# Kernel optimization log

Hardware: AMD Instinct MI355X
Metric: run time of the kernel (lower is better)

Reference implementation:

```python
import math
import jax, jax.numpy as jnp
import numpy as np

SPECIAL = 4; LABEL_ID = 3
ACT_V = 64; TIME_V = 32
VOCAB = SPECIAL + ACT_V + TIME_V  # 100
D = 1024; L = 4; H = 16; DH = D // H
B = 4; T = 1024
CAT0, CAT1 = 16, 32
N_NUM = 4; N_TIME = 6


def _posenc(t, d):
    pos = np.arange(t)[:, None]
    i = np.arange(d // 2)[None, :]
    ang = pos / np.power(10000.0, 2.0 * i / d)
    pe = np.zeros((t, d), dtype=np.float32)
    pe[:, 0::2] = np.sin(ang)
    pe[:, 1::2] = np.cos(ang)
    return jnp.asarray(pe)


def _ln(x, g, b):
    m = jnp.mean(x, -1, keepdims=True)
    v = jnp.mean((x - m) ** 2, -1, keepdims=True)
    return (x - m) * jax.lax.rsqrt(v + 1e-5) * g + b


def setup_inputs() -> dict:
    key = jax.random.key(0)
    ks = iter(jax.random.split(key, 64))
    nrm = lambda shape, s=0.02: jax.random.normal(next(ks), shape, jnp.float32) * s
    inp = {}
    inp['tokens'] = jax.random.randint(next(ks), (B, T), 0, VOCAB)
    inp['cat_feats'] = jax.random.randint(next(ks), (B, T, 2), 0, CAT0)
    inp['num_feats'] = jax.random.normal(next(ks), (B, T, N_NUM), jnp.float32)
    inp['time_feats'] = jax.random.normal(next(ks), (B, T, N_TIME), jnp.float32)
    inp['attention_mask'] = jnp.ones((B, T), jnp.int32)
    inp['loss_mask'] = jax.random.randint(next(ks), (B, T), 0, 2).astype(bool)
    inp['task_ids'] = jax.random.randint(next(ks), (B,), 0, 2)
    # embedder params
    inp['E'] = nrm((VOCAB, D))
    inp['cat_emb0'] = nrm((CAT0, D))
    inp['cat_emb1'] = nrm((CAT1, D))
    inp['Wn'] = nrm((N_NUM, D)); inp['bn'] = jnp.zeros((D,), jnp.float32)
    inp['Wt'] = nrm((N_TIME, D)); inp['bt'] = jnp.zeros((D,), jnp.float32)
    # backbone params, stacked over layers
    inp['Wqkv'] = nrm((L, D, 3 * D)); inp['bqkv'] = jnp.zeros((L, 3 * D), jnp.float32)
    inp['Wo'] = nrm((L, D, D)); inp['bo'] = jnp.zeros((L, D), jnp.float32)
    inp['ln1_g'] = jnp.ones((L, D), jnp.float32); inp['ln1_b'] = jnp.zeros((L, D), jnp.float32)
    inp['W1'] = nrm((L, D, 4 * D)); inp['b1'] = jnp.zeros((L, 4 * D), jnp.float32)
    inp['W2'] = nrm((L, 4 * D, D)); inp['b2'] = jnp.zeros((L, D), jnp.float32)
    inp['ln2_g'] = jnp.ones((L, D), jnp.float32); inp['ln2_b'] = jnp.zeros((L, D), jnp.float32)
    inp['lnf_g'] = jnp.ones((D,), jnp.float32); inp['lnf_b'] = jnp.zeros((D,), jnp.float32)
    # heads
    inp['W_next'] = nrm((D, ACT_V)); inp['b_next'] = jnp.zeros((ACT_V,), jnp.float32)
    inp['W_timeh'] = nrm((D, TIME_V)); inp['b_timeh'] = jnp.zeros((TIME_V,), jnp.float32)
    inp['task_embed'] = nrm((2, D))
    inp['tied_scale_act'] = jnp.asarray(0.5, jnp.float32)
    inp['tied_scale_time'] = jnp.asarray(0.5, jnp.float32)
    inp['copy_scale_act'] = jnp.asarray(0.5, jnp.float32)
    inp['copy_scale_time'] = jnp.asarray(0.5, jnp.float32)
    return inp


def reference(tokens, cat_feats, num_feats, time_feats, attention_mask, loss_mask, task_ids,
              E, cat_emb0, cat_emb1, Wn, bn, Wt, bt,
              Wqkv, bqkv, Wo, bo, ln1_g, ln1_b, W1, b1, W2, b2, ln2_g, ln2_b, lnf_g, lnf_b,
              W_next, b_next, W_timeh, b_timeh, task_embed,
              tied_scale_act, tied_scale_time, copy_scale_act, copy_scale_time):
    Bq, Tq = tokens.shape
    # ---- EventEmbedder: sum of token/categorical/numeric/time embeddings + PE
    x = E[tokens] + cat_emb0[cat_feats[..., 0]] + cat_emb1[cat_feats[..., 1]]
    x = x + num_feats @ Wn + bn + time_feats @ Wt + bt
    x = x + _posenc(Tq, D)
    # ---- task conditioning
    x = x + task_embed[task_ids][:, None, :]
    # ---- causal + key-padding mask
    pad = attention_mask == 0
    causal = jnp.triu(jnp.ones((Tq, Tq), bool), 1)
    neg = jnp.where(causal[None, None] | pad[:, None, None, :], -1e9, 0.0).astype(x.dtype)
    # ---- pre-LN decoder-only transformer
    for l in range(L):
        hln = _ln(x, ln1_g[l], ln1_b[l])
        qkv = hln @ Wqkv[l] + bqkv[l]
        q, k, v = jnp.split(qkv, 3, axis=-1)
        q = q.reshape(Bq, Tq, H, DH); k = k.reshape(Bq, Tq, H, DH); v = v.reshape(Bq, Tq, H, DH)
        sc = jnp.einsum('bqhd,bkhd->bhqk', q, k) / math.sqrt(DH) + neg
        p = jax.nn.softmax(sc, axis=-1)
        a = jnp.einsum('bhqk,bkhd->bqhd', p, v).reshape(Bq, Tq, D)
        x = x + a @ Wo[l] + bo[l]
        hln = _ln(x, ln2_g[l], ln2_b[l])
        x = x + jax.nn.relu(hln @ W1[l] + b1[l]) @ W2[l] + b2[l]
    h = _ln(x, lnf_g, lnf_b)  # [B,T,D]
    # ---- parametric heads
    param_next = h @ W_next + b_next
    param_time = h @ W_timeh + b_timeh
    # ---- weight-tied heads
    W_act = E[SPECIAL:SPECIAL + ACT_V]
    W_tb = E[SPECIAL + ACT_V:SPECIAL + ACT_V + TIME_V]
    tied_act = h @ W_act.T
    tied_time = h @ W_tb.T
    # ---- retrieval/copy head (vectorized gather-matmul-scatter)
    is_label = tokens == LABEL_ID
    value_mask = jnp.pad(is_label[:, :-1], ((0, 0), (1, 0)))  # prev token is <LABEL>
    act_start = SPECIAL; time_start = SPECIAL + ACT_V
    val_act = value_mask & (tokens >= act_start) & (tokens < time_start)
    val_time = value_mask & (tokens >= time_start) & (tokens < time_start + TIME_V)
    sims = jnp.einsum('bqd,bkd->bqk', h, h) / math.sqrt(D)  # all-pairs similarity
    oh_act = jax.nn.one_hot(tokens - act_start, ACT_V, dtype=h.dtype) * val_act[..., None]
    oh_time = jax.nn.one_hot(tokens - time_start, TIME_V, dtype=h.dtype) * val_time[..., None]
    qm = loss_mask[..., None].astype(h.dtype)  # copy logits only at query <LABEL> positions
    copy_act = jnp.einsum('bqk,bkc->bqc', sims, oh_act) * qm
    copy_time = jnp.einsum('bqk,bkc->bqc', sims, oh_time) * qm
    sp = jax.nn.softplus
    activity_logits = param_next + sp(tied_scale_act) * tied_act + sp(copy_scale_act) * copy_act
    time_logits = param_time + sp(tied_scale_time) * tied_time + sp(copy_scale_time) * copy_time
    return activity_logits, time_logits
```

## Files before the change

### kernel.cpp

```cpp
#include <hip/hip_runtime.h>
#include <cstdint>
#include <cstddef>

typedef unsigned short u16;
typedef __attribute__((ext_vector_type(8))) short bf16x8;
typedef __attribute__((ext_vector_type(4))) float f32x4;

#define DMODEL 1024
#define TLEN   1024
#define BATCH  4
#define NHEAD  16

__device__ __forceinline__ float bf2f(u16 u) {
  union { unsigned int i; float f; } x; x.i = ((unsigned int)u) << 16; return x.f;
}
__device__ __forceinline__ u16 f2bf(float f) {
  union { float f; unsigned int i; } x; x.f = f;
  unsigned int r = x.i + 0x7fffu + ((x.i >> 16) & 1u);
  return (u16)(r >> 16);
}
__device__ __forceinline__ void ld8bf(const u16* p, float* f) {
  uint4 u = *(const uint4*)p;
  f[0] = bf2f((u16)(u.x & 0xffff)); f[1] = bf2f((u16)(u.x >> 16));
  f[2] = bf2f((u16)(u.y & 0xffff)); f[3] = bf2f((u16)(u.y >> 16));
  f[4] = bf2f((u16)(u.z & 0xffff)); f[5] = bf2f((u16)(u.z >> 16));
  f[6] = bf2f((u16)(u.w & 0xffff)); f[7] = bf2f((u16)(u.w >> 16));
}
__device__ __forceinline__ void ld4bf(const u16* p, float* f) {
  uint2 u = *(const uint2*)p;
  f[0] = bf2f((u16)(u.x & 0xffff)); f[1] = bf2f((u16)(u.x >> 16));
  f[2] = bf2f((u16)(u.y & 0xffff)); f[3] = bf2f((u16)(u.y >> 16));
}
__device__ __forceinline__ float softplus_f(float x) {
  return (x > 20.f) ? x : log1pf(__expf(x));
}
__device__ __forceinline__ void async_ld16(const void* g, void* l) {
  __builtin_amdgcn_global_load_lds(
      (const __attribute__((address_space(1))) unsigned int*)g,
      (__attribute__((address_space(3))) unsigned int*)l, 16, 0, 0);
}

__global__ void embed_kernel(const int* __restrict__ tokens, const int* __restrict__ cat,
    const float* __restrict__ numf, const float* __restrict__ timef, const int* __restrict__ task_ids,
    const float* __restrict__ E, const float* __restrict__ ce0, const float* __restrict__ ce1,
    const float* __restrict__ Wn, const float* __restrict__ bn, const float* __restrict__ Wtm,
    const float* __restrict__ btm, const float* __restrict__ taskemb, float* __restrict__ X)
{
  const int bt = blockIdx.x;
  const int b = bt >> 10, t = bt & 1023;
  const int tok = tokens[bt];
  const int c0 = cat[bt * 2 + 0], c1 = cat[bt * 2 + 1];
  const int tk = task_ids[b];
  float nf[4], tf[6];
#pragma unroll
  for (int i = 0; i < 4; ++i) nf[i] = numf[bt * 4 + i];
#pragma unroll
  for (int i = 0; i < 6; ++i) tf[i] = timef[bt * 6 + i];
  const int d0 = threadIdx.x * 4;
  float v[4];
  {
    float4 a = *(const float4*)(E + (size_t)tok * DMODEL + d0);
    float4 b2 = *(const float4*)(ce0 + (size_t)c0 * DMODEL + d0);
    float4 c2 = *(const float4*)(ce1 + (size_t)c1 * DMODEL + d0);
    float4 d2 = *(const float4*)(taskemb + (size_t)tk * DMODEL + d0);
    float4 e2 = *(const float4*)(bn + d0);
    float4 f2 = *(const float4*)(btm + d0);
    v[0] = a.x + b2.x + c2.x + d2.x + e2.x + f2.x;
    v[1] = a.y + b2.y + c2.y + d2.y + e2.y + f2.y;
    v[2] = a.z + b2.z + c2.z + d2.z + e2.z + f2.z;
    v[3] = a.w + b2.w + c2.w + d2.w + e2.w + f2.w;
  }
#pragma unroll
  for (int i = 0; i < 4; ++i) {
    float4 w = *(const float4*)(Wn + (size_t)i * DMODEL + d0);
    v[0] += nf[i] * w.x; v[1] += nf[i] * w.y; v[2] += nf[i] * w.z; v[3] += nf[i] * w.w;
  }
#pragma unroll
  for (int i = 0; i < 6; ++i) {
    float4 w = *(const float4*)(Wtm + (size_t)i * DMODEL + d0);
    v[0] += tf[i] * w.x; v[1] += tf[i] * w.y; v[2] += tf[i] * w.z; v[3] += tf[i] * w.w;
  }
#pragma unroll
  for (int j = 0; j < 4; ++j) {
    const int d = d0 + j;
    const int i2 = d >> 1;
    const float ang = (float)t * expf(-0.017988946f * (float)i2);
    v[j] += (d & 1) ? cosf(ang) : sinf(ang);
  }
  *(float4*)(X + (size_t)bt * DMODEL + d0) = make_float4(v[0], v[1], v[2], v[3]);
}

__global__ void ln_kernel(const float* __restrict__ X, const float* __restrict__ g,
                          const float* __restrict__ be, u16* __restrict__ O)
{
  const int row = blockIdx.x * 4 + (threadIdx.x >> 6);
  const int lane = threadIdx.x & 63;
  const float* xr = X + (size_t)row * DMODEL;
  float v[16];
  float s = 0.f, s2 = 0.f;
#pragma unroll
  for (int i = 0; i < 4; ++i) {
    float4 t4 = *(const float4*)(xr + lane * 4 + i * 256);
    v[i*4+0] = t4.x; v[i*4+1] = t4.y; v[i*4+2] = t4.z; v[i*4+3] = t4.w;
    s  += t4.x + t4.y + t4.z + t4.w;
    s2 += t4.x*t4.x + t4.y*t4.y + t4.z*t4.z + t4.w*t4.w;
  }
#pragma unroll
  for (int off = 32; off > 0; off >>= 1) {
    s  += __shfl_xor(s, off, 64);
    s2 += __shfl_xor(s2, off, 64);
  }
  const float mean = s * (1.f / 1024.f);
  const float var  = s2 * (1.f / 1024.f) - mean * mean;
  const float rs   = rsqrtf(var + 1e-5f);
  u16* orow = O + (size_t)row * DMODEL;
#pragma unroll
  for (int i = 0; i < 4; ++i) {
    float4 gg = *(const float4*)(g + lane * 4 + i * 256);
    float4 bb = *(const float4*)(be + lane * 4 + i * 256);
    float r0 = (v[i*4+0] - mean) * rs * gg.x + bb.x;
    float r1 = (v[i*4+1] - mean) * rs * gg.y + bb.y;
    float r2 = (v[i*4+2] - mean) * rs * gg.z + bb.z;
    float r3 = (v[i*4+3] - mean) * rs * gg.w + bb.w;
    uint2 o2;
    o2.x = (unsigned)f2bf(r0) | ((unsigned)f2bf(r1) << 16);
    o2.y = (unsigned)f2bf(r2) | ((unsigned)f2bf(r3) << 16);
    *(uint2*)(orow + lane * 4 + i * 256) = o2;
  }
}

__global__ void transpose_f2b(const float* __restrict__ in, u16* __restrict__ out,
                              int R, int C, int ldin)
{
  __shared__ u16 tile[64][65];
  const int c0 = blockIdx.x * 64, r0 = blockIdx.y * 64;
  const int tx = threadIdx.x & 15, ty = threadIdx.x >> 4;
#pragma unroll
  for (int i = 0; i < 4; ++i) {
    const int r = ty + i * 16;
    float4 f = *(const float4*)(in + (size_t)(r0 + r) * ldin + c0 + tx * 4);
    tile[r][tx*4+0] = f2bf(f.x);
    tile[r][tx*4+1] = f2bf(f.y);
    tile[r][tx*4+2] = f2bf(f.z);
    tile[r][tx*4+3] = f2bf(f.w);
  }
  __syncthreads();
#pragma unroll
  for (int i = 0; i < 4; ++i) {
    const int rr = ty + i * 16;
    uint2 o;
    o.x = (unsigned)tile[tx*4+0][rr] | ((unsigned)tile[tx*4+1][rr] << 16);
    o.y = (unsigned)tile[tx*4+2][rr] | ((unsigned)tile[tx*4+3][rr] << 16);
    *(uint2*)(out + (size_t)(c0 + rr) * R + r0 + tx * 4) = o;
  }
}

template<bool RESID, bool RELU, bool OUTBF>
__global__ void gemm_bt(const u16* __restrict__ A, const u16* __restrict__ Bt,
                        const float* __restrict__ bias, const float* __restrict__ resid,
                        void* __restrict__ outp, int M, int N, int K, int lda)
{
  __shared__ u16 As[128 * 32];
  __shared__ u16 Bs[128 * 32];
  const int tid = threadIdx.x;
  const int wave = tid >> 6, lane = tid & 63;
  const int m0 = blockIdx.y * 128, n0 = blockIdx.x * 128;
  const int wm = (wave >> 1) * 64, wn = (wave & 1) * 64;
  const int lrow = lane & 15, quad = lane >> 4;
  f32x4 acc[4][4] = {};
  for (int kt = 0; kt < K; kt += 32) {
    __syncthreads();
#pragma unroll
    for (int p = 0; p < 2; ++p) {
      const int idx = p * 256 + tid;
      const int r = idx >> 2, cc = (idx & 3) << 3;
      const int lofs = (p * 256 + wave * 64) << 3;
      async_ld16(A + (size_t)(m0 + r) * lda + kt + cc, As + lofs);
      async_ld16(Bt + (size_t)(n0 + r) * K + kt + cc, Bs + lofs);
    }
    __syncthreads();
    bf16x8 af[4], bfr[4];
#pragma unroll
    for (int i = 0; i < 4; ++i) {
      af[i]  = *(const bf16x8*)(As + (wm + i * 16 + lrow) * 32 + quad * 8);
      bfr[i] = *(const bf16x8*)(Bs + (wn + i * 16 + lrow) * 32 + quad * 8);
    }
#pragma unroll
    for (int i = 0; i < 4; ++i)
#pragma unroll
      for (int j = 0; j < 4; ++j)
        acc[i][j] = __builtin_amdgcn_mfma_f32_16x16x32_bf16(af[i], bfr[j], acc[i][j], 0, 0, 0);
  }
#pragma unroll
  for (int i = 0; i < 4; ++i) {
#pragma unroll
    for (int j = 0; j < 4; ++j) {
      const int col = n0 + wn + j * 16 + lrow;
      const float bv = bias ? bias[col] : 0.f;
#pragma unroll
      for (int r = 0; r < 4; ++r) {
        const int row = m0 + wm + i * 16 + quad * 4 + r;
        float vv = acc[i][j][r] + bv;
        if (RESID) vv += resid[(size_t)row * N + col];
        if (RELU)  vv = fmaxf(vv, 0.f);
        if (OUTBF) ((u16*)outp)[(size_t)row * N + col] = f2bf(vv);
        else       ((float*)outp)[(size_t)row * N + col] = vv;
      }
    }
  }
}

__launch_bounds__(256, 4)
__global__ void attn_flash(u16* __restrict__ QKV, const int* __restrict__ amask)
{
  __shared__ u16 Pw[4][16 * 72];
  const int tid  = threadIdx.x;
  const int wave = tid >> 6, lane = tid & 63;
  const int l15  = lane & 15, quad = lane >> 4;
  const int qb = blockIdx.x, h = blockIdx.y, b = blockIdx.z;
  const int qbase = qb * 64 + wave * 16;

  u16* bq = QKV + (size_t)b * TLEN * 3072 + h * 64;
  const u16* Kb = bq + 1024;
  const u16* Vb = bq + 2048;
  const int* am = amask + b * TLEN;

  bf16x8 aq0 = *(const bf16x8*)(bq + (size_t)(qbase + l15) * 3072 + quad * 8);
  bf16x8 aq1 = *(const bf16x8*)(bq + (size_t)(qbase + l15) * 3072 + 32 + quad * 8);

  f32x4 o[4] = {};
  float m[4], l[4];
#pragma unroll
  for (int r = 0; r < 4; ++r) { m[r] = -1e30f; l[r] = 0.f; }

  u16* myP = Pw[wave];

  for (int kb = 0; kb <= qb; ++kb) {
    const int kt = kb * 64;
    float p[4][4];
#pragma unroll
    for (int j = 0; j < 4; ++j) {
      const u16* kr = Kb + (size_t)(kt + j * 16 + l15) * 3072;
      bf16x8 bk0 = *(const bf16x8*)(kr + quad * 8);
      bf16x8 bk1 = *(const bf16x8*)(kr + 32 + quad * 8);
      f32x4 sacc = {};
      sacc = __builtin_amdgcn_mfma_f32_16x16x32_bf16(aq0, bk0, sacc, 0, 0, 0);
      sacc = __builtin_amdgcn_mfma_f32_16x16x32_bf16(aq1, bk1, sacc, 0, 0, 0);
      const float negm = (am[kt + j * 16 + l15] == 0) ? -1e9f : 0.f;
#pragma unroll
      for (int r = 0; r < 4; ++r) p[j][r] = sacc[r] * 0.125f + negm;
    }
    if (kb == qb) {
#pragma unroll
      for (int j = 0; j < 4; ++j) {
        const int colL = j * 16 + l15;
#pragma unroll
        for (int r = 0; r < 4; ++r) {
          const int rowL = wave * 16 + quad * 4 + r;
          if (colL > rowL) p[j][r] = -1e30f;
        }
      }
    }
#pragma unroll
    for (int r = 0; r < 4; ++r) {
      float mm = fmaxf(fmaxf(p[0][r], p[1][r]), fmaxf(p[2][r], p[3][r]));
      mm = fmaxf(mm, __shfl_xor(mm, 1));
      mm = fmaxf(mm, __shfl_xor(mm, 2));
      mm = fmaxf(mm, __shfl_xor(mm, 4));
      mm = fmaxf(mm, __shfl_xor(mm, 8));
      const float nm = fmaxf(m[r], mm);
      const float al = __expf(m[r] - nm);
      m[r] = nm;
      float ls = 0.f;
#pragma unroll
      for (int j = 0; j < 4; ++j) { p[j][r] = __expf(p[j][r] - nm); ls += p[j][r]; }
      ls += __shfl_xor(ls, 1); ls += __shfl_xor(ls, 2);
      ls += __shfl_xor(ls, 4); ls += __shfl_xor(ls, 8);
      l[r] = l[r] * al + ls;
#pragma unroll
      for (int n = 0; n < 4; ++n) o[n][r] *= al;
    }
#pragma unroll
    for (int j = 0; j < 4; ++j)
#pragma unroll
      for (int r = 0; r < 4; ++r)
        myP[(quad * 4 + r) * 72 + j * 16 + l15] = f2bf(p[j][r]);
    __asm__ volatile("s_waitcnt lgkmcnt(0)" ::: "memory");
    bf16x8 pa0 = *(const bf16x8*)(myP + l15 * 72 + quad * 8);
    bf16x8 pa1 = *(const bf16x8*)(myP + l15 * 72 + 32 + quad * 8);
#pragma unroll
    for (int n = 0; n < 4; ++n) {
      const u16* vcol = Vb + n * 16 + l15;
#pragma unroll
      for (int c = 0; c < 2; ++c) {
        bf16x8 bv;
        short* pv = (short*)&bv;
#pragma unroll
        for (int jj = 0; jj < 8; ++jj)
          pv[jj] = (short)vcol[(size_t)(kt + c * 32 + quad * 8 + jj) * 3072];
        o[n] = __builtin_amdgcn_mfma_f32_16x16x32_bf16(c == 0 ? pa0 : pa1, bv, o[n], 0, 0, 0);
      }
    }
  }
#pragma unroll
  for (int r = 0; r < 4; ++r) {
    const float inv = (l[r] > 0.f) ? 1.f / l[r] : 0.f;
    u16* po = bq + (size_t)(qbase + quad * 4 + r) * 3072;
#pragma unroll
    for (int n = 0; n < 4; ++n)
      po[n * 16 + l15] = f2bf(o[n][r] * inv);
  }
}

__global__ void foldM(const float* __restrict__ E, const float* __restrict__ Wnext,
                      const float* __restrict__ Wtimeh, const float* __restrict__ bnext,
                      const float* __restrict__ btimeh, const float* __restrict__ s_act,
                      const float* __restrict__ s_time, u16* __restrict__ MT, float* __restrict__ biasC)
{
  const int c = blockIdx.x;
  const float sa = softplus_f(s_act[0]);
  const float st = softplus_f(s_time[0]);
  const int d0 = threadIdx.x * 4;
#pragma unroll
  for (int j = 0; j < 4; ++j) {
    const int d = d0 + j;
    float v = 0.f;
    if (c < 64)      v = Wnext[(size_t)d * 64 + c] + sa * E[(size_t)(4 + c) * DMODEL + d];
    else if (c < 96) v = Wtimeh[(size_t)d * 32 + (c - 64)] + st * E[(size_t)(68 + c - 64) * DMODEL + d];
    MT[(size_t)c * DMODEL + d] = f2bf(v);
  }
  if (threadIdx.x == 0) {
    float bv = 0.f;
    if (c < 64) bv = bnext[c];
    else if (c < 96) bv = btimeh[c - 64];
    biasC[c] = bv;
  }
}

__global__ void gbuild(const int* __restrict__ tokens, const u16* __restrict__ HB,
                       float* __restrict__ G, int* __restrict__ Gnz)
{
  const int b = blockIdx.x;
  __shared__ int cls[1024];
  for (int i = threadIdx.x; i < 96 * 1024; i += 256) G[(size_t)b * 96 * 1024 + i] = 0.f;
  for (int k = threadIdx.x; k < 1024; k += 256) {
    int c = -1;
    if (k > 0 && tokens[b * 1024 + k - 1] == 3) {
      const int tok = tokens[b * 1024 + k];
      if (tok >= 4 && tok < 68) c = tok - 4;
      else if (tok >= 68 && tok < 100) c = 64 + (tok - 68);
    }
    cls[k] = c;
  }
  if (threadIdx.x < 96) Gnz[b * 96 + threadIdx.x] = 0;
  __syncthreads();
  const int d0 = threadIdx.x * 4;
  for (int k = 1; k < 1024; ++k) {
    const int c = cls[k];
    if (c < 0) continue;
    if (threadIdx.x == 0) Gnz[b * 96 + c] = 1;
    float* gr = G + ((size_t)b * 96 + c) * 1024 + d0;
    float hv[4];
    ld4bf(HB + ((size_t)b * 1024 + k) * 1024 + d0, hv);
#pragma unroll
    for (int j = 0; j < 4; ++j) gr[j] += hv[j];
  }
}

__global__ void final_kernel(const u16* __restrict__ HB, const float* __restrict__ OUT96,
                             const float* __restrict__ G, const int* __restrict__ Gnz,
                             const int* __restrict__ lossm, const float* __restrict__ s_ca,
                             const float* __restrict__ s_ct, float* __restrict__ out_act,
                             float* __restrict__ out_time)
{
  __shared__ float hs[1024];
  const int row = blockIdx.x;
  const int b = row >> 10;
  const u16* hrow = HB + (size_t)row * 1024;
  {
    const int i = threadIdx.x;
    float hv[8];
    ld8bf(hrow + i * 8, hv);
#pragma unroll
    for (int j = 0; j < 8; ++j) hs[i * 8 + j] = hv[j];
  }
  __syncthreads();
  const int c = threadIdx.x;
  if (c >= 96) return;
  float val = OUT96[(size_t)row * 128 + c];
  if (lossm[row] != 0 && Gnz[b * 96 + c] != 0) {
    const float4* gr = (const float4*)(G + ((size_t)b * 96 + c) * 1024);
    float dot = 0.f;
    for (int d4 = 0; d4 < 256; ++d4) {
      float4 gg = gr[d4];
      dot += hs[d4*4+0]*gg.x + hs[d4*4+1]*gg.y + hs[d4*4+2]*gg.z + hs[d4*4+3]*gg.w;
    }
    const float sc = (c < 64) ? softplus_f(s_ca[0]) : softplus_f(s_ct[0]);
    val += sc * dot * (1.f / 32.f);
  }
  if (c < 64) out_act[(size_t)row * 64 + c] = val;
  else        out_time[(size_t)row * 32 + (c - 64)] = val;
}

extern "C" void kernel_launch(void* const* d_in, const int* in_sizes, int n_in,
                              void* d_out, int out_size, void* d_ws, size_t ws_size,
                              hipStream_t stream)
{
  const int*   tokens = (const int*)d_in[0];
  const int*   cat    = (const int*)d_in[1];
  const float* numf   = (const float*)d_in[2];
  const float* timef  = (const float*)d_in[3];
  const int*   amask  = (const int*)d_in[4];
  const int*   lossm  = (const int*)d_in[5];
  const int*   task   = (const int*)d_in[6];
  const float* E      = (const float*)d_in[7];
  const float* ce0    = (const float*)d_in[8];
  const float* ce1    = (const float*)d_in[9];
  const float* Wn     = (const float*)d_in[10];
  const float* bn     = (const float*)d_in[11];
  const float* Wtm    = (const float*)d_in[12];
  const float* btm    = (const float*)d_in[13];
  const float* Wqkv   = (const float*)d_in[14];
  const float* bqkv   = (const float*)d_in[15];
  const float* Wo     = (const float*)d_in[16];
  const float* bo     = (const float*)d_in[17];
  const float* ln1g   = (const float*)d_in[18];
  const float* ln1b   = (const float*)d_in[19];
  const float* W1     = (const float*)d_in[20];
  const float* b1     = (const float*)d_in[21];
  const float* W2     = (const float*)d_in[22];
  const float* b2     = (const float*)d_in[23];
  const float* ln2g   = (const float*)d_in[24];
  const float* ln2b   = (const float*)d_in[25];
  const float* lnfg   = (const float*)d_in[26];
  const float* lnfb   = (const float*)d_in[27];
  const float* Wnext  = (const float*)d_in[28];
  const float* bnext  = (const float*)d_in[29];
  const float* Wtimeh = (const float*)d_in[30];
  const float* btimeh = (const float*)d_in[31];
  const float* taskemb= (const float*)d_in[32];
  const float* ts_act = (const float*)d_in[33];
  const float* ts_time= (const float*)d_in[34];
  const float* cs_act = (const float*)d_in[35];
  const float* cs_time= (const float*)d_in[36];

  float* out_act  = (float*)d_out;
  float* out_time = out_act + (size_t)BATCH * TLEN * 64;

  uint8_t* ws = (uint8_t*)d_ws;
  float* X   = (float*)(ws);
  u16*   XB  = (u16*)(ws + (16ull << 20));
  u16*   SCR = (u16*)(ws + (24ull << 20));
  u16*   WT  = (u16*)(ws + (48ull << 20));
  u16*   MT    = (u16*)  (ws + (24ull << 20));
  float* BIASC = (float*)(ws + (24ull << 20) + (512ull << 10));
  float* OUT96 = (float*)(ws + (25ull << 20));
  float* G     = (float*)(ws + (28ull << 20));
  int*   GNZ   = (int*)  (ws + (30ull << 20));

  embed_kernel<<<4096, 256, 0, stream>>>(tokens, cat, numf, timef, task, E, ce0, ce1,
                                         Wn, bn, Wtm, btm, taskemb, X);

  for (int l = 0; l < 4; ++l) {
    ln_kernel<<<1024, 256, 0, stream>>>(X, ln1g + l * 1024, ln1b + l * 1024, XB);
    transpose_f2b<<<dim3(48, 16), 256, 0, stream>>>(Wqkv + (size_t)l * 1024 * 3072, WT, 1024, 3072, 3072);
    gemm_bt<false, false, true><<<dim3(24, 32), 256, 0, stream>>>(XB, WT, bqkv + l * 3072, nullptr, SCR, 4096, 3072, 1024, 1024);
    attn_flash<<<dim3(16, 16, 4), 256, 0, stream>>>(SCR, amask);
    transpose_f2b<<<dim3(16, 16), 256, 0, stream>>>(Wo + (size_t)l * 1024 * 1024, WT, 1024, 1024, 1024);
    gemm_bt<true, false, false><<<dim3(8, 32), 256, 0, stream>>>(SCR , WT, bo + l * 1024, X, X, 4096, 1024, 1024, 3072);
    ln_kernel<<<1024, 256, 0, stream>>>(X, ln2g + l * 1024, ln2b + l * 1024, XB);
    for (int nh = 0; nh < 2; ++nh) {
      transpose_f2b<<<dim3(32, 16), 256, 0, stream>>>(W1 + (size_t)l * 1024 * 4096 + nh * 2048, WT, 1024, 2048, 4096);
      gemm_bt<false, true, true><<<dim3(16, 32), 256, 0, stream>>>(XB, WT, b1 + l * 4096 + nh * 2048, nullptr, SCR, 4096, 2048, 1024, 1024);
      transpose_f2b<<<dim3(16, 32), 256, 0, stream>>>(W2 + ((size_t)l * 4096 + nh * 2048) * 1024, WT, 2048, 1024, 1024);
      gemm_bt<true, false, false><<<dim3(8, 32), 256, 0, stream>>>(SCR, WT, nh == 0 ? (b2 + l * 1024) : nullptr, X, X, 4096, 1024, 2048, 2048);
    }
  }

  ln_kernel<<<1024, 256, 0, stream>>>(X, lnfg, lnfb, XB);
  foldM<<<128, 256, 0, stream>>>(E, Wnext, Wtimeh, bnext, btimeh, ts_act, ts_time, MT, BIASC);
  gemm_bt<false, false, false><<<dim3(1, 32), 256, 0, stream>>>(XB, MT, BIASC, nullptr, OUT96, 4096, 128, 1024, 1024);
  gbuild<<<4, 256, 0, stream>>>(tokens, XB, G, GNZ);
  final_kernel<<<4096, 128, 0, stream>>>(XB, OUT96, G, GNZ, lossm, cs_act, cs_time, out_act, out_time);
}
```

Baseline: 1.842 ms.

## Write V transposed from QKV GEMM epilogue for vectorized attention loads

```diff
diff --git a/kernel.cpp b/kernel.cpp
--- a/kernel.cpp
+++ b/kernel.cpp
@@ -155,10 +155,11 @@
   }
 }
 
-template<bool RESID, bool RELU, bool OUTBF>
+template<bool RESID, bool RELU, bool OUTBF, bool QKVMODE>
 __global__ void gemm_bt(const u16* __restrict__ A, const u16* __restrict__ Bt,
                         const float* __restrict__ bias, const float* __restrict__ resid,
-                        void* __restrict__ outp, int M, int N, int K, int lda)
+                        void* __restrict__ outp, u16* __restrict__ vt,
+                        int M, int N, int K, int lda)
 {
   __shared__ u16 As[128 * 32];
   __shared__ u16 Bs[128 * 32];
@@ -203,15 +204,27 @@
         float vv = acc[i][j][r] + bv;
         if (RESID) vv += resid[(size_t)row * N + col];
         if (RELU)  vv = fmaxf(vv, 0.f);
-        if (OUTBF) ((u16*)outp)[(size_t)row * N + col] = f2bf(vv);
-        else       ((float*)outp)[(size_t)row * N + col] = vv;
+        if (QKVMODE) {
+          if (col < 2048) {
+            ((u16*)outp)[(size_t)row * 2048 + col] = f2bf(vv);
+          } else {
+            const int hd = col - 2048;
+            const int b = row >> 10, t = row & 1023;
+            vt[(((size_t)b * 16 + (hd >> 6)) * 64 + (hd & 63)) * 1024 + t] = f2bf(vv);
+          }
+        } else if (OUTBF) {
+          ((u16*)outp)[(size_t)row * N + col] = f2bf(vv);
+        } else {
+          ((float*)outp)[(size_t)row * N + col] = vv;
+        }
       }
     }
   }
 }
 
 __launch_bounds__(256, 4)
-__global__ void attn_flash(u16* __restrict__ QKV, const int* __restrict__ amask)
+__global__ void attn_flash(u16* __restrict__ QK, const u16* __restrict__ VT,
+                           const int* __restrict__ amask)
 {
   __shared__ u16 Pw[4][16 * 72];
   const int tid  = threadIdx.x;
@@ -220,13 +233,13 @@
   const int qb = blockIdx.x, h = blockIdx.y, b = blockIdx.z;
   const int qbase = qb * 64 + wave * 16;
 
-  u16* bq = QKV + (size_t)b * TLEN * 3072 + h * 64;
+  u16* bq = QK + (size_t)b * TLEN * 2048 + h * 64;
   const u16* Kb = bq + 1024;
-  const u16* Vb = bq + 2048;
+  const u16* Vb = VT + ((size_t)b * 16 + h) * 64 * 1024;
   const int* am = amask + b * TLEN;
 
-  bf16x8 aq0 = *(const bf16x8*)(bq + (size_t)(qbase + l15) * 3072 + quad * 8);
-  bf16x8 aq1 = *(const bf16x8*)(bq + (size_t)(qbase + l15) * 3072 + 32 + quad * 8);
+  bf16x8 aq0 = *(const bf16x8*)(bq + (size_t)(qbase + l15) * 2048 + quad * 8);
+  bf16x8 aq1 = *(const bf16x8*)(bq + (size_t)(qbase + l15) * 2048 + 32 + quad * 8);
 
   f32x4 o[4] = {};
   float m[4], l[4];
@@ -240,7 +253,7 @@
     float p[4][4];
 #pragma unroll
     for (int j = 0; j < 4; ++j) {
-      const u16* kr = Kb + (size_t)(kt + j * 16 + l15) * 3072;
+      const u16* kr = Kb + (size_t)(kt + j * 16 + l15) * 2048;
       bf16x8 bk0 = *(const bf16x8*)(kr + quad * 8);
       bf16x8 bk1 = *(const bf16x8*)(kr + 32 + quad * 8);
       f32x4 sacc = {};
@@ -290,22 +303,17 @@
     bf16x8 pa1 = *(const bf16x8*)(myP + l15 * 72 + 32 + quad * 8);
 #pragma unroll
     for (int n = 0; n < 4; ++n) {
-      const u16* vcol = Vb + n * 16 + l15;
-#pragma unroll
-      for (int c = 0; c < 2; ++c) {
-        bf16x8 bv;
-        short* pv = (short*)&bv;
-#pragma unroll
-        for (int jj = 0; jj < 8; ++jj)
-          pv[jj] = (short)vcol[(size_t)(kt + c * 32 + quad * 8 + jj) * 3072];
-        o[n] = __builtin_amdgcn_mfma_f32_16x16x32_bf16(c == 0 ? pa0 : pa1, bv, o[n], 0, 0, 0);
-      }
+      const u16* vrow = Vb + (size_t)(n * 16 + l15) * 1024 + kt;
+      bf16x8 bv0 = *(const bf16x8*)(vrow + quad * 8);
+      bf16x8 bv1 = *(const bf16x8*)(vrow + 32 + quad * 8);
+      o[n] = __builtin_amdgcn_mfma_f32_16x16x32_bf16(pa0, bv0, o[n], 0, 0, 0);
+      o[n] = __builtin_amdgcn_mfma_f32_16x16x32_bf16(pa1, bv1, o[n], 0, 0, 0);
     }
   }
 #pragma unroll
   for (int r = 0; r < 4; ++r) {
     const float inv = (l[r] > 0.f) ? 1.f / l[r] : 0.f;
-    u16* po = bq + (size_t)(qbase + quad * 4 + r) * 3072;
+    u16* po = bq + (size_t)(qbase + quad * 4 + r) * 2048;
 #pragma unroll
     for (int n = 0; n < 4; ++n)
       po[n * 16 + l15] = f2bf(o[n][r] * inv);
@@ -451,6 +459,7 @@
   float* X   = (float*)(ws);
   u16*   XB  = (u16*)(ws + (16ull << 20));
   u16*   SCR = (u16*)(ws + (24ull << 20));
+  u16*   VT  = (u16*)(ws + (40ull << 20));
   u16*   WT  = (u16*)(ws + (48ull << 20));
   u16*   MT    = (u16*)  (ws + (24ull << 20));
   float* BIASC = (float*)(ws + (24ull << 20) + (512ull << 10));
@@ -464,22 +473,22 @@
   for (int l = 0; l < 4; ++l) {
     ln_kernel<<<1024, 256, 0, stream>>>(X, ln1g + l * 1024, ln1b + l * 1024, XB);
     transpose_f2b<<<dim3(48, 16), 256, 0, stream>>>(Wqkv + (size_t)l * 1024 * 3072, WT, 1024, 3072, 3072);
-    gemm_bt<false, false, true><<<dim3(24, 32), 256, 0, stream>>>(XB, WT, bqkv + l * 3072, nullptr, SCR, 4096, 3072, 1024, 1024);
-    attn_flash<<<dim3(16, 16, 4), 256, 0, stream>>>(SCR, amask);
+    gemm_bt<false, false, true, true><<<dim3(24, 32), 256, 0, stream>>>(XB, WT, bqkv + l * 3072, nullptr, SCR, VT, 4096, 3072, 1024, 1024);
+    attn_flash<<<dim3(16, 16, 4), 256, 0, stream>>>(SCR, VT, amask);
     transpose_f2b<<<dim3(16, 16), 256, 0, stream>>>(Wo + (size_t)l * 1024 * 1024, WT, 1024, 1024, 1024);
-    gemm_bt<true, false, false><<<dim3(8, 32), 256, 0, stream>>>(SCR , WT, bo + l * 1024, X, X, 4096, 1024, 1024, 3072);
+    gemm_bt<true, false, false, false><<<dim3(8, 32), 256, 0, stream>>>(SCR , WT, bo + l * 1024, X, X, nullptr, 4096, 1024, 1024, 2048);
     ln_kernel<<<1024, 256, 0, stream>>>(X, ln2g + l * 1024, ln2b + l * 1024, XB);
     for (int nh = 0; nh < 2; ++nh) {
       transpose_f2b<<<dim3(32, 16), 256, 0, stream>>>(W1 + (size_t)l * 1024 * 4096 + nh * 2048, WT, 1024, 2048, 4096);
-      gemm_bt<false, true, true><<<dim3(16, 32), 256, 0, stream>>>(XB, WT, b1 + l * 4096 + nh * 2048, nullptr, SCR, 4096, 2048, 1024, 1024);
+      gemm_bt<false, true, true, false><<<dim3(16, 32), 256, 0, stream>>>(XB, WT, b1 + l * 4096 + nh * 2048, nullptr, SCR, nullptr, 4096, 2048, 1024, 1024);
       transpose_f2b<<<dim3(16, 32), 256, 0, stream>>>(W2 + ((size_t)l * 4096 + nh * 2048) * 1024, WT, 2048, 1024, 1024);
-      gemm_bt<true, false, false><<<dim3(8, 32), 256, 0, stream>>>(SCR, WT, nh == 0 ? (b2 + l * 1024) : nullptr, X, X, 4096, 1024, 2048, 2048);
+      gemm_bt<true, false, false, false><<<dim3(8, 32), 256, 0, stream>>>(SCR, WT, nh == 0 ? (b2 + l * 1024) : nullptr, X, X, nullptr, 4096, 1024, 2048, 2048);
     }
   }
 
   ln_kernel<<<1024, 256, 0, stream>>>(X, lnfg, lnfb, XB);
   foldM<<<128, 256, 0, stream>>>(E, Wnext, Wtimeh, bnext, btimeh, ts_act, ts_time, MT, BIASC);
-  gemm_bt<false, false, false><<<dim3(1, 32), 256, 0, stream>>>(XB, MT, BIASC, nullptr, OUT96, 4096, 128, 1024, 1024);
+  gemm_bt<false, false, false, false><<<dim3(1, 32), 256, 0, stream>>>(XB, MT, BIASC, nullptr, OUT96, nullptr, 4096, 128, 1024, 1024);
   gbuild<<<4, 256, 0, stream>>>(tokens, XB, G, GNZ);
   final_kernel<<<4096, 128, 0, stream>>>(XB, OUT96, G, GNZ, lossm, cs_act, cs_time, out_act, out_time);
 }
```

Measured after the change: 1.873 ms. About the same (+1.7%).
